# Kernel optimization log

Measured on AMD Instinct MI355X. Metric: run time of the kernel, lower is better.

The kernel has to match this reference:

```python
import jax, jax.numpy as jnp
import numpy as np

COST_CLASS, COST_BBOX, COST_GIOU = 1.0, 5.0, 2.0


def _box_area(b):
    return (b[..., 2] - b[..., 0]) * (b[..., 3] - b[..., 1])


def _generalized_box_iou(b1, b2):
    # b1: (B,Q,4), b2: (B,N,4), xyxy -> (B,Q,N)
    a1 = _box_area(b1)[:, :, None]
    a2 = _box_area(b2)[:, None, :]
    lt = jnp.maximum(b1[:, :, None, :2], b2[:, None, :, :2])
    rb = jnp.minimum(b1[:, :, None, 2:], b2[:, None, :, 2:])
    wh = jnp.clip(rb - lt, 0.0)
    inter = wh[..., 0] * wh[..., 1]
    union = a1 + a2 - inter
    iou = inter / union
    lt_c = jnp.minimum(b1[:, :, None, :2], b2[:, None, :, :2])
    rb_c = jnp.maximum(b1[:, :, None, 2:], b2[:, None, :, 2:])
    wh_c = jnp.clip(rb_c - lt_c, 0.0)
    area_c = wh_c[..., 0] * wh_c[..., 1]
    return iou - (area_c - union) / area_c


@jax.jit
def _cost_matrix(pred_logits, pred_boxes, tgt_labels, tgt_boxes):
    B, Q, _ = pred_logits.shape
    N = tgt_labels.shape[1]
    out_prob = jax.nn.softmax(pred_logits, axis=-1)  # (B,Q,C+1)
    idx = jnp.broadcast_to(tgt_labels[:, None, :], (B, Q, N))
    cost_class = -jnp.take_along_axis(out_prob, idx, axis=-1)          # (B,Q,N)
    cost_bbox = jnp.abs(pred_boxes[:, :, None, :] - tgt_boxes[:, None, :, :]).sum(-1)  # L1 cdist
    cost_giou = -_generalized_box_iou(pred_boxes, tgt_boxes)
    return COST_CLASS * cost_class + COST_BBOX * cost_bbox + COST_GIOU * cost_giou


def _lsa(cost):
    """Shortest-augmenting-path Hungarian (Jonker-Volgenant style).
    cost: (n, m) with n <= m. Returns col4row[i] = assigned column of row i.
    Matches scipy.optimize.linear_sum_assignment (minimization)."""
    n, m = cost.shape
    INF = np.inf
    u = np.zeros(n + 1)
    v = np.zeros(m + 1)
    p = np.zeros(m + 1, dtype=np.int64)   # p[j] = row (1-indexed) assigned to col j
    way = np.zeros(m + 1, dtype=np.int64)
    for i in range(1, n + 1):
        p[0] = i
        j0 = 0
        minv = np.full(m + 1, INF)
        used = np.zeros(m + 1, dtype=bool)
        while True:
            used[j0] = True
            i0 = p[j0]
            cur = cost[i0 - 1] - u[i0] - v[1:]
            free = ~used[1:]
            upd = free & (cur < minv[1:])
            minv[1:][upd] = cur[upd]
            way[1:][upd] = j0
            cand = np.where(free, minv[1:], INF)
            j1 = int(np.argmin(cand)) + 1
            delta = cand[j1 - 1]
            uj = np.nonzero(used)[0]
            u[p[uj]] += delta
            v[uj] -= delta
            minv[~used] -= delta
            j0 = j1
            if p[j0] == 0:
                break
        while j0 != 0:
            j1 = way[j0]
            p[j0] = p[j1]
            j0 = j1
    col4row = np.zeros(n, dtype=np.int64)
    for j in range(1, m + 1):
        if p[j] != 0:
            col4row[p[j] - 1] = j - 1
    return col4row


def setup_inputs() -> dict:
    key = jax.random.key(0)
    k1, k2, k3, k4, k5 = jax.random.split(key, 5)
    B, Q, N, C1 = 64, 600, 80, 92

    def make_boxes(kx, ky, shape):
        xy = jax.random.uniform(kx, shape + (2,)) * 0.6
        wh = jax.random.uniform(ky, shape + (2,)) * 0.35 + 0.02
        return jnp.concatenate([xy, xy + wh], axis=-1)  # valid xyxy

    pred_logits = jax.random.normal(k1, (B, Q, C1), dtype=jnp.float32)
    pred_boxes = make_boxes(k2, k3, (B, Q))
    tgt_labels = jax.random.randint(k4, (B, N), 0, 91)
    tgt_boxes = make_boxes(k5, jax.random.fold_in(k5, 1), (B, N))
    return {"pred_logits": pred_logits, "pred_boxes": pred_boxes,
            "tgt_labels": tgt_labels, "tgt_boxes": tgt_boxes}


def reference(pred_logits, pred_boxes, tgt_labels, tgt_boxes):
    # Batched cost-matrix build on device, then host Hungarian per sample
    # (mirrors the original's .cpu().numpy() + scipy linear_sum_assignment).
    C = np.asarray(_cost_matrix(pred_logits, pred_boxes, tgt_labels, tgt_boxes))  # (B,Q,N)
    B, Q, N = C.shape
    rows = np.empty((B, N), dtype=np.int64)
    cols = np.empty((B, N), dtype=np.int64)
    for b in range(B):
        q_of_t = _lsa(C[b].T)              # transpose: N <= Q; query index per target
        order = np.argsort(q_of_t, kind="stable")
        rows[b] = q_of_t[order]            # sorted query (row) indices
        cols[b] = order                    # matching target (col) indices
    return jnp.asarray(rows), jnp.asarray(cols)
```

## Files before the change

kernel.cpp:

```cpp
#include <hip/hip_runtime.h>
#include <math.h>

#define BB 64
#define QQ 600
#define NT 80
#define NC 92
#define SLOTS 10
#define NTILE 10
#define NTHR 256
#define NWAVE 4
#define MAXROUNDS 16
#define STALLCAP 3
#define SPINCAP (1 << 20)
#define MAGIC 0x5A17C0DE


template <int CTRL>
__device__ __forceinline__ int dppi(int x) {
    return __builtin_amdgcn_update_dpp(x, x, CTRL, 0xF, 0xF, false);
}

__device__ __forceinline__ unsigned wave_min_u32(unsigned x) {
    unsigned y;
    y = (unsigned)dppi<0x121>((int)x); x = x < y ? x : y;
    y = (unsigned)dppi<0x122>((int)x); x = x < y ? x : y;
    y = (unsigned)dppi<0x124>((int)x); x = x < y ? x : y;
    y = (unsigned)dppi<0x128>((int)x); x = x < y ? x : y;
    y = (unsigned)__builtin_amdgcn_ds_swizzle((int)x, 0x401F); x = x < y ? x : y;
    y = (unsigned)__shfl_xor((int)x, 32); x = x < y ? x : y;
    return x;
}

__device__ __forceinline__ unsigned long long u64min(unsigned long long a,
                                                     unsigned long long b) {
    return a < b ? a : b;
}

__device__ __forceinline__ unsigned long long wave_min_u64(unsigned long long x) {
    union U { unsigned long long v; int i[2]; };
    U c, o; c.v = x;
    o.i[0] = dppi<0x121>(c.i[0]); o.i[1] = dppi<0x121>(c.i[1]); c.v = u64min(c.v, o.v);
    o.i[0] = dppi<0x122>(c.i[0]); o.i[1] = dppi<0x122>(c.i[1]); c.v = u64min(c.v, o.v);
    o.i[0] = dppi<0x124>(c.i[0]); o.i[1] = dppi<0x124>(c.i[1]); c.v = u64min(c.v, o.v);
    o.i[0] = dppi<0x128>(c.i[0]); o.i[1] = dppi<0x128>(c.i[1]); c.v = u64min(c.v, o.v);
    o.i[0] = __builtin_amdgcn_ds_swizzle(c.i[0], 0x401F);
    o.i[1] = __builtin_amdgcn_ds_swizzle(c.i[1], 0x401F); c.v = u64min(c.v, o.v);
    o.i[0] = __shfl_xor(c.i[0], 32);
    o.i[1] = __shfl_xor(c.i[1], 32);                       c.v = u64min(c.v, o.v);
    return c.v;
}

__device__ __forceinline__ unsigned f32_key(float f) {
    unsigned b = __float_as_uint(f);
    return b ^ ((unsigned)((int)b >> 31) | 0x80000000u);
}
__device__ __forceinline__ float key_f32(unsigned k) {
    unsigned b = (k & 0x80000000u) ? (k ^ 0x80000000u) : ~k;
    return __uint_as_float(b);
}
__device__ __forceinline__ unsigned long long f64_key(double d) {
    unsigned long long b = (unsigned long long)__double_as_longlong(d);
    return b ^ ((unsigned long long)((long long)b >> 63) | 0x8000000000000000ULL);
}
__device__ __forceinline__ double key_f64(unsigned long long k) {
    unsigned long long b = (k & 0x8000000000000000ULL) ? (k ^ 0x8000000000000000ULL) : ~k;
    return __longlong_as_double((long long)b);
}

__global__ __launch_bounds__(256) void matcher_kernel(
    const float* __restrict__ logits,
    const float* __restrict__ pboxes,
    const int*   __restrict__ tlabels,
    const float* __restrict__ tboxes,
    float* __restrict__ cost,
    float* __restrict__ pm1,
    float* __restrict__ pm2,
    int*   __restrict__ pmj,
    int*   __restrict__ done,
    int* __restrict__ rows_out,
    int* __restrict__ cols_out)
{
    __shared__ float tile[64 * 93];
    __shared__ float s_m[64], s_s[64];
    __shared__ float s_tb[NT * 4];
    __shared__ int   s_tl[NT];
    __shared__ double vA[QQ];
    __shared__ double u[NT];
    __shared__ double bidm1[NT], bidm2[NT];
    __shared__ int    bidj[NT], bidver[NT];
    __shared__ int    pA[QQ];
    __shared__ int    verA[QQ];
    __shared__ int    colrow[QQ];
    __shared__ int    assigned[NT];
    __shared__ int    plist[NT];
    __shared__ int    pcnt;
    __shared__ int    wayA[QQ];
    __shared__ int    c4r[NT];
    __shared__ int    djkA[NT];

    const int g   = blockIdx.x;
    const int b   = g / NTILE;
    const int tix = g % NTILE;
    const int tid = threadIdx.x;
    const int qq  = tid & 63;
    const int wv  = tid >> 6;
    const float* C = cost + (size_t)b * NT * QQ;

    {
        const int q0 = tix * 64;
        const int nq = min(64, QQ - q0);
        const float* src = logits + ((size_t)b * QQ + q0) * NC;
        for (int idx = tid; idx < nq * NC; idx += 256) {
            const int r = idx / NC;
            tile[r * 93 + (idx - r * NC)] = src[idx];
        }
        for (int i = tid; i < NT * 4; i += 256) s_tb[i] = tboxes[b * NT * 4 + i];
        for (int i = tid; i < NT;     i += 256) s_tl[i] = tlabels[b * NT + i];
        __syncthreads();

        if (tid < nq) {
            const float* r = &tile[tid * 93];
            float m0 = r[0], m1 = r[1], m2 = r[2], m3 = r[3];
            for (int c = 4; c < NC; c += 4) {
                m0 = fmaxf(m0, r[c]);   m1 = fmaxf(m1, r[c+1]);
                m2 = fmaxf(m2, r[c+2]); m3 = fmaxf(m3, r[c+3]);
            }
            const float m = fmaxf(fmaxf(m0, m1), fmaxf(m2, m3));
            float s0 = 0.f, s1 = 0.f, s2 = 0.f, s3 = 0.f;
            for (int c = 0; c < NC; c += 4) {
                s0 += expf(r[c]   - m); s1 += expf(r[c+1] - m);
                s2 += expf(r[c+2] - m); s3 += expf(r[c+3] - m);
            }
            s_m[tid] = m; s_s[tid] = (s0 + s1) + (s2 + s3);
        }
        __syncthreads();

        const bool valid = qq < nq;
        float px1 = 0.f, py1 = 0.f, px2 = 0.f, py2 = 0.f, pa = 0.f, m = 0.f, s = 1.f;
        if (valid) {
            const float* pb = pboxes + ((size_t)b * QQ + q0 + qq) * 4;
            px1 = pb[0]; py1 = pb[1]; px2 = pb[2]; py2 = pb[3];
            pa  = (px2 - px1) * (py2 - py1);
            m = s_m[qq]; s = s_s[qq];
        }
        float* crow = cost + (size_t)b * NT * QQ + q0 + qq;

        for (int tt = 0; tt < 20; ++tt) {
            const int t = wv * 20 + tt;
            float costv = INFINITY;
            if (valid) {
                const int lbl = s_tl[t];
                const float cc = -(expf(tile[qq * 93 + lbl] - m) / s);
                const float tx1 = s_tb[t*4+0], ty1 = s_tb[t*4+1];
                const float tx2 = s_tb[t*4+2], ty2 = s_tb[t*4+3];
                const float cb = fabsf(px1-tx1) + fabsf(py1-ty1)
                               + fabsf(px2-tx2) + fabsf(py2-ty2);
                const float ta = (tx2 - tx1) * (ty2 - ty1);
                const float iw = fmaxf(fminf(px2, tx2) - fmaxf(px1, tx1), 0.f);
                const float ih = fmaxf(fminf(py2, ty2) - fmaxf(py1, ty1), 0.f);
                const float inter = iw * ih;
                const float uni   = pa + ta - inter;
                const float iou   = inter / uni;
                const float cw = fmaxf(fmaxf(px2, tx2) - fminf(px1, tx1), 0.f);
                const float ch = fmaxf(fmaxf(py2, ty2) - fminf(py1, ty1), 0.f);
                const float ac = cw * ch;
                const float giou = iou - (ac - uni) / ac;
                costv = (1.0f * cc + 5.0f * cb) + 2.0f * (-giou);
                crow[(size_t)t * QQ] = costv;
            }
            const unsigned key  = f32_key(costv);
            const unsigned kmin = wave_min_u32(key);
            const unsigned long long tied = __ballot(key == kmin);
            const int winlane = __builtin_ctzll(tied);
            const unsigned cand = (qq == winlane) ? 0xFFFFFFFFu : key;
            const unsigned k2   = wave_min_u32(cand);
            if (qq == 0) {
                const size_t idx = ((size_t)b * NT + t) * NTILE + tix;
                pm1[idx] = key_f32(kmin); pm2[idx] = key_f32(k2);
                pmj[idx] = q0 + winlane;
            }
        }
    }
    __syncthreads();
    if (tid == 0)
        __hip_atomic_store(&done[b * 16 + tix], MAGIC, __ATOMIC_RELEASE, __HIP_MEMORY_SCOPE_AGENT);
    if (tix != 0) return;

    if (tid < NTILE) {
        int spins = 0;
        while (__hip_atomic_load(&done[b * 16 + tid], __ATOMIC_ACQUIRE, __HIP_MEMORY_SCOPE_AGENT) != MAGIC) {
            __builtin_amdgcn_s_sleep(8);
            if (++spins > SPINCAP) break;
        }
    }
    __syncthreads();

    for (int c = tid; c < QQ; c += NTHR) { pA[c] = -1; verA[c] = 0; vA[c] = 0.0; }
    if (tid < NT) { assigned[tid] = 0; bidver[tid] = 0; }
    __syncthreads();

    if (tid < NT) {
        const int t = tid;
        const float* p1 = pm1 + ((size_t)b * NT + t) * NTILE;
        const float* p2 = pm2 + ((size_t)b * NT + t) * NTILE;
        const int*   pj = pmj + ((size_t)b * NT + t) * NTILE;
        float m1 = INFINITY, m2 = INFINITY; int j1 = QQ;
        for (int k = 0; k < NTILE; ++k) {
            const float a1 = p1[k], a2 = p2[k];
            const int   aj = pj[k];
            if (a1 < m1) { m2 = fminf(m1, a2); m1 = a1; j1 = aj; }
            else         { m2 = fminf(m2, a1); }
        }
        bidm1[t] = (double)m1; bidm2[t] = (double)m2; bidj[t] = j1;
        u[t] = (double)m1;
    }
    __syncthreads();

    int prev_np = 0x7fffffff, stall = 0;
    for (int round = 0; round < MAXROUNDS; ++round) {
        for (int c = tid; c < QQ; c += NTHR) colrow[c] = 0x7fffffff;
        if (tid == 0) pcnt = 0;
        __syncthreads();
        if (tid < NT && !assigned[tid]) {
            const int j = bidj[tid];
            if (bidver[tid] == verA[j]) atomicMin(&colrow[j], tid);
        }
        __syncthreads();
        if (tid < NT && !assigned[tid]) {
            const int i = tid, j = bidj[i];
            if (bidver[i] == verA[j] && colrow[j] == i) {
                const double m1 = bidm1[i], m2 = bidm2[i];
                const int prev = pA[j];
                pA[j] = i;
                verA[j] = verA[j] + 1;
                vA[j] -= (m2 - m1);
                u[i] = m2;
                assigned[i] = 1;
                if (prev >= 0) assigned[prev] = 0;
            }
        }
        __syncthreads();
        if (tid < NT && !assigned[tid]) { const int k = atomicAdd(&pcnt, 1); plist[k] = tid; }
        __syncthreads();
        const int np = pcnt;
        if (np == 0) break;
        if (np >= prev_np) { if (++stall >= STALLCAP) break; }
        else               { stall = 0; }
        prev_np = np;
        for (int idx = wv; idx < np; idx += NWAVE) {
            const int i = plist[idx];
            const float* rp = C + (size_t)i * QQ;
            float rowv[SLOTS];
            #pragma unroll
            for (int k = 0; k < SLOTS; ++k) { const int c = qq + 64*k; rowv[k] = (c < QQ) ? rp[c] : 0.f; }
            double m1 = INFINITY, m2 = INFINITY; int j1 = QQ;
            #pragma unroll
            for (int k = 0; k < SLOTS; ++k) {
                const int c = qq + 64 * k;
                if (c < QQ) {
                    const double key = (double)rowv[k] - vA[c];
                    if (key < m1)      { m2 = m1; m1 = key; j1 = c; }
                    else if (key < m2) { m2 = key; }
                }
            }
            const unsigned long long k1 = f64_key(m1);
            const unsigned long long kminv = wave_min_u64(k1);
            const unsigned long long tied = __ballot(k1 == kminv);
            const int winlane = __builtin_ctzll(tied);
            const unsigned long long c2 = (qq == winlane) ? f64_key(m2) : k1;
            const unsigned long long k2minv = wave_min_u64(c2);
            const int jwin = __shfl(j1, winlane);
            if (qq == 0) {
                bidm1[i] = key_f64(kminv); bidm2[i] = key_f64(k2minv); bidj[i] = jwin;
                bidver[i] = verA[jwin];
                u[i] = key_f64(kminv);
            }
        }
        __syncthreads();
    }

    if (wv != 0) return;
    const int lane = qq;

    int nd = 0;
    for (int i = 0; i < NT; ++i) {
        if (!assigned[i]) { if (lane == 0) djkA[nd] = i; ++nd; }
    }

    double v_[SLOTS], minv_[SLOTS];
    int p_[SLOTS];
    #pragma unroll
    for (int k = 0; k < SLOTS; ++k) {
        const int c = lane + 64 * k;
        v_[k] = (c < QQ) ? vA[c] : 0.0;
        p_[k] = (c < QQ) ? pA[c] : -1;
    }

    float rowv[SLOTS];
    for (int ii = 0; ii < nd; ++ii) {
        const int i = djkA[ii];
        #pragma unroll
        for (int k = 0; k < SLOTS; ++k) minv_[k] = INFINITY;
        unsigned usedm = 0;
        int j0 = -1;
        double ui0 = u[i];
        {
            const float* rp = C + (size_t)i * QQ;
            #pragma unroll
            for (int k = 0; k < SLOTS; ++k) { const int c = lane + 64*k; rowv[k] = (c < QQ) ? rp[c] : 0.f; }
        }
        int j1, i1;

        for (;;) {
            if (j0 >= 0 && (j0 & 63) == lane) usedm |= 1u << (j0 >> 6);

            double bestv = INFINITY; int bestc = QQ;
            #pragma unroll
            for (int k = 0; k < SLOTS; ++k) {
                const int c = lane + 64 * k;
                if (c < QQ && !((usedm >> k) & 1u)) {
                    const double cur = ((double)rowv[k] - ui0) - v_[k];
                    if (cur < minv_[k]) { minv_[k] = cur; wayA[c] = j0; }
                    if (minv_[k] < bestv) { bestv = minv_[k]; bestc = c; }
                }
            }
            const unsigned long long kb = f64_key(bestv);
            const unsigned long long kminv = wave_min_u64(kb);
            const unsigned long long tied = __ballot(kb == kminv);
            const int winlane = __builtin_ctzll(tied);
            const double delta = key_f64(kminv);
            j1 = __shfl(bestc, winlane);

            {
                const int slot = j1 >> 6, lj = j1 & 63;
                int myp = p_[0];
                #pragma unroll
                for (int k = 1; k < SLOTS; ++k) if (slot == k) myp = p_[k];
                i1 = __shfl(myp, lj);
            }

            double ui_next = 0.0;
            float rown[SLOTS];
            if (i1 >= 0) {
                ui_next = u[i1];
                const float* rp = C + (size_t)i1 * QQ;
                #pragma unroll
                for (int k = 0; k < SLOTS; ++k) { const int c = lane + 64*k; rown[k] = (c < QQ) ? rp[c] : 0.f; }
            }

            #pragma unroll
            for (int k = 0; k < SLOTS; ++k) {
                const int c = lane + 64 * k;
                if (c < QQ) {
                    if ((usedm >> k) & 1u) { v_[k] -= delta; u[p_[k]] += delta; }
                    else                     minv_[k] -= delta;
                }
            }
            if (lane == 0) u[i] += delta;

            j0 = j1;
            if (i1 < 0) break;
            ui0 = ui_next;
            #pragma unroll
            for (int k = 0; k < SLOTS; ++k) rowv[k] = rown[k];
        }

        if (lane == 0) {
            int jj = j1;
            while (jj >= 0) {
                const int pr = wayA[jj];
                pA[jj] = (pr < 0) ? i : pA[pr];
                jj = pr;
            }
        }
        #pragma unroll
        for (int k = 0; k < SLOTS; ++k) {
            const int c = lane + 64 * k;
            p_[k] = (c < QQ) ? pA[c] : -1;
        }
    }

    #pragma unroll
    for (int k = 0; k < SLOTS; ++k) {
        const int c = lane + 64 * k;
        if (c < QQ) { const int t = pA[c]; if (t >= 0) c4r[t] = c; }
    }
    for (int t = lane; t < NT; t += 64) {
        const int c = c4r[t];
        int rank = 0;
        for (int t2 = 0; t2 < NT; ++t2) rank += (c4r[t2] < c) ? 1 : 0;
        rows_out[b * NT + rank] = c;
        cols_out[b * NT + rank] = t;
    }
}

extern "C" void kernel_launch(void* const* d_in, const int* in_sizes, int n_in,
                              void* d_out, int out_size, void* d_ws, size_t ws_size,
                              hipStream_t stream) {
    (void)in_sizes; (void)n_in; (void)out_size; (void)ws_size;
    const float* logits  = (const float*)d_in[0];
    const float* pboxes  = (const float*)d_in[1];
    const int*   tlabels = (const int*)d_in[2];
    const float* tboxes  = (const float*)d_in[3];
    float* cost = (float*)d_ws;
    float* pm1  = cost + (size_t)BB * NT * QQ;
    float* pm2  = pm1  + (size_t)BB * NT * NTILE;
    int*   pmj  = (int*)(pm2 + (size_t)BB * NT * NTILE);
    int*   done = pmj + (size_t)BB * NT * NTILE;
    int*   out  = (int*)d_out;

    matcher_kernel<<<dim3(BB * NTILE), NTHR, 0, stream>>>(
        logits, pboxes, tlabels, tboxes, cost, pm1, pm2, pmj, done,
        out, out + BB * NT);
}
```

Before: 121.8 us.

## Cache hot cost rows in LDS and parallelize softmax across waves

The softmax max and sum now run over four waves, each covering 23 of the classes, and the exponentials are stored back in the tile so the class cost becomes a single multiply. After the cost phase, the freed logits tile is reused as an LDS cache holding up to nine cost rows, so the auction rounds and Dijkstra augmentation read those rows from LDS instead of global memory. The auction drops its per-round colrow reset and plist compaction in favour of round-tagged atomicMin keys and __syncthreads_count. The cache adds atomics and shared stores on misses, and the cache slot is read without a barrier, which risks races between waves.

```diff
diff --git a/kernel.cpp b/kernel.cpp
--- a/kernel.cpp
+++ b/kernel.cpp
@@ -11,6 +11,7 @@
 #define NWAVE 4
 #define MAXROUNDS 16
 #define STALLCAP 3
+#define NCAP 9
 #define SPINCAP (1 << 20)
 #define MAGIC 0x5A17C0DE
 
@@ -81,7 +82,7 @@
     int* __restrict__ cols_out)
 {
     __shared__ float tile[64 * 93];
-    __shared__ float s_m[64], s_s[64];
+    __shared__ float s_pm[4 * 64], s_ps[4 * 64];
     __shared__ float s_tb[NT * 4];
     __shared__ int   s_tl[NT];
     __shared__ double vA[QQ];
@@ -92,11 +93,11 @@
     __shared__ int    verA[QQ];
     __shared__ int    colrow[QQ];
     __shared__ int    assigned[NT];
-    __shared__ int    plist[NT];
-    __shared__ int    pcnt;
     __shared__ int    wayA[QQ];
     __shared__ int    c4r[NT];
     __shared__ int    djkA[NT];
+    __shared__ int    cslot[NT];
+    __shared__ int    ncache;
 
     const int g   = blockIdx.x;
     const int b   = g / NTILE;
@@ -105,6 +106,7 @@
     const int qq  = tid & 63;
     const int wv  = tid >> 6;
     const float* C = cost + (size_t)b * NT * QQ;
+    float* const cacheF = tile;
 
     {
         const int q0 = tix * 64;
@@ -118,30 +120,39 @@
         for (int i = tid; i < NT;     i += 256) s_tl[i] = tlabels[b * NT + i];
         __syncthreads();
 
-        if (tid < nq) {
-            const float* r = &tile[tid * 93];
-            float m0 = r[0], m1 = r[1], m2 = r[2], m3 = r[3];
-            for (int c = 4; c < NC; c += 4) {
-                m0 = fmaxf(m0, r[c]);   m1 = fmaxf(m1, r[c+1]);
-                m2 = fmaxf(m2, r[c+2]); m3 = fmaxf(m3, r[c+3]);
-            }
-            const float m = fmaxf(fmaxf(m0, m1), fmaxf(m2, m3));
-            float s0 = 0.f, s1 = 0.f, s2 = 0.f, s3 = 0.f;
-            for (int c = 0; c < NC; c += 4) {
-                s0 += expf(r[c]   - m); s1 += expf(r[c+1] - m);
-                s2 += expf(r[c+2] - m); s3 += expf(r[c+3] - m);
-            }
-            s_m[tid] = m; s_s[tid] = (s0 + s1) + (s2 + s3);
+        {
+            const int c0 = wv * 23;
+            const float* r = &tile[qq * 93];
+            float pm = r[c0];
+            #pragma unroll 11
+            for (int c = 1; c < 23; ++c) pm = fmaxf(pm, r[c0 + c]);
+            s_pm[wv * 64 + qq] = pm;
+        }
+        __syncthreads();
+        {
+            const int c0 = wv * 23;
+            float* r = &tile[qq * 93];
+            const float m = fmaxf(fmaxf(s_pm[qq], s_pm[64 + qq]),
+                                  fmaxf(s_pm[128 + qq], s_pm[192 + qq]));
+            float sum = 0.f;
+            #pragma unroll 11
+            for (int c = 0; c < 23; ++c) {
+                const float e = expf(r[c0 + c] - m);
+                r[c0 + c] = e;
+                sum += e;
+            }
+            s_ps[wv * 64 + qq] = sum;
         }
         __syncthreads();
 
         const bool valid = qq < nq;
-        float px1 = 0.f, py1 = 0.f, px2 = 0.f, py2 = 0.f, pa = 0.f, m = 0.f, s = 1.f;
+        float px1 = 0.f, py1 = 0.f, px2 = 0.f, py2 = 0.f, pa = 0.f, inv_s = 1.f;
         if (valid) {
             const float* pb = pboxes + ((size_t)b * QQ + q0 + qq) * 4;
             px1 = pb[0]; py1 = pb[1]; px2 = pb[2]; py2 = pb[3];
             pa  = (px2 - px1) * (py2 - py1);
-            m = s_m[qq]; s = s_s[qq];
+            const float s = (s_ps[qq] + s_ps[64 + qq]) + (s_ps[128 + qq] + s_ps[192 + qq]);
+            inv_s = 1.f / s;
         }
         float* crow = cost + (size_t)b * NT * QQ + q0 + qq;
 
@@ -150,7 +161,7 @@
             float costv = INFINITY;
             if (valid) {
                 const int lbl = s_tl[t];
-                const float cc = -(expf(tile[qq * 93 + lbl] - m) / s);
+                const float cc = -(tile[qq * 93 + lbl] * inv_s);
                 const float tx1 = s_tb[t*4+0], ty1 = s_tb[t*4+1];
                 const float tx2 = s_tb[t*4+2], ty2 = s_tb[t*4+3];
                 const float cb = fabsf(px1-tx1) + fabsf(py1-ty1)
@@ -195,8 +206,9 @@
     }
     __syncthreads();
 
-    for (int c = tid; c < QQ; c += NTHR) { pA[c] = -1; verA[c] = 0; vA[c] = 0.0; }
-    if (tid < NT) { assigned[tid] = 0; bidver[tid] = 0; }
+    for (int c = tid; c < QQ; c += NTHR) { pA[c] = -1; verA[c] = 0; vA[c] = 0.0; colrow[c] = 0x7fffffff; }
+    if (tid < NT) { assigned[tid] = 0; bidver[tid] = 0; cslot[tid] = -1; }
+    if (tid == 0) ncache = 0;
     __syncthreads();
 
     if (tid < NT) {
@@ -216,19 +228,47 @@
     }
     __syncthreads();
 
+#define FETCH_ROW(dst, i)                                                      \
+    do {                                                                       \
+        const int _cs = cslot[i];                                              \
+        if (_cs >= 0) {                                                        \
+            _Pragma("unroll")                                                  \
+            for (int k = 0; k < SLOTS; ++k) {                                  \
+                const int c = qq + 64 * k;                                     \
+                dst[k] = (c < QQ) ? cacheF[_cs * QQ + c] : 0.f;                \
+            }                                                                  \
+        } else {                                                               \
+            const float* _rp = C + (size_t)(i) * QQ;                           \
+            _Pragma("unroll")                                                  \
+            for (int k = 0; k < SLOTS; ++k) {                                  \
+                const int c = qq + 64 * k;                                     \
+                dst[k] = (c < QQ) ? _rp[c] : 0.f;                              \
+            }                                                                  \
+            int _slot = 0;                                                     \
+            if (qq == 0) _slot = atomicAdd(&ncache, 1);                        \
+            _slot = __shfl(_slot, 0);                                          \
+            if (_slot < NCAP) {                                                \
+                _Pragma("unroll")                                              \
+                for (int k = 0; k < SLOTS; ++k) {                              \
+                    const int c = qq + 64 * k;                                 \
+                    if (c < QQ) cacheF[_slot * QQ + c] = dst[k];               \
+                }                                                              \
+                if (qq == 0) cslot[i] = _slot;                                 \
+            }                                                                  \
+        }                                                                      \
+    } while (0)
+
     int prev_np = 0x7fffffff, stall = 0;
     for (int round = 0; round < MAXROUNDS; ++round) {
-        for (int c = tid; c < QQ; c += NTHR) colrow[c] = 0x7fffffff;
-        if (tid == 0) pcnt = 0;
-        __syncthreads();
+        const int rkey = (MAXROUNDS - round) << 7;
         if (tid < NT && !assigned[tid]) {
             const int j = bidj[tid];
-            if (bidver[tid] == verA[j]) atomicMin(&colrow[j], tid);
+            if (bidver[tid] == verA[j]) atomicMin(&colrow[j], rkey | tid);
         }
         __syncthreads();
         if (tid < NT && !assigned[tid]) {
             const int i = tid, j = bidj[i];
-            if (bidver[i] == verA[j] && colrow[j] == i) {
+            if (bidver[i] == verA[j] && colrow[j] == (rkey | i)) {
                 const double m1 = bidm1[i], m2 = bidm2[i];
                 const int prev = pA[j];
                 pA[j] = i;
@@ -240,19 +280,15 @@
             }
         }
         __syncthreads();
-        if (tid < NT && !assigned[tid]) { const int k = atomicAdd(&pcnt, 1); plist[k] = tid; }
-        __syncthreads();
-        const int np = pcnt;
+        const int np = __syncthreads_count(tid < NT && !assigned[tid]);
         if (np == 0) break;
         if (np >= prev_np) { if (++stall >= STALLCAP) break; }
         else               { stall = 0; }
         prev_np = np;
-        for (int idx = wv; idx < np; idx += NWAVE) {
-            const int i = plist[idx];
-            const float* rp = C + (size_t)i * QQ;
+        for (int i = wv; i < NT; i += NWAVE) {
+            if (assigned[i]) continue;
             float rowv[SLOTS];
-            #pragma unroll
-            for (int k = 0; k < SLOTS; ++k) { const int c = qq + 64*k; rowv[k] = (c < QQ) ? rp[c] : 0.f; }
+            FETCH_ROW(rowv, i);
             double m1 = INFINITY, m2 = INFINITY; int j1 = QQ;
             #pragma unroll
             for (int k = 0; k < SLOTS; ++k) {
@@ -304,11 +340,7 @@
         unsigned usedm = 0;
         int j0 = -1;
         double ui0 = u[i];
-        {
-            const float* rp = C + (size_t)i * QQ;
-            #pragma unroll
-            for (int k = 0; k < SLOTS; ++k) { const int c = lane + 64*k; rowv[k] = (c < QQ) ? rp[c] : 0.f; }
-        }
+        FETCH_ROW(rowv, i);
         int j1, i1;
 
         for (;;) {
@@ -343,9 +375,7 @@
             float rown[SLOTS];
             if (i1 >= 0) {
                 ui_next = u[i1];
-                const float* rp = C + (size_t)i1 * QQ;
-                #pragma unroll
-                for (int k = 0; k < SLOTS; ++k) { const int c = lane + 64*k; rown[k] = (c < QQ) ? rp[c] : 0.f; }
+                FETCH_ROW(rown, i1);
             }
 
             #pragma unroll
```

Result: slower. 131.1 us (+7.6%).
